# Kernel optimization log

Measured on AMD Instinct MI355X. Metric: run time of the kernel, lower is better.

Reference implementation:

```python
import jax, jax.numpy as jnp
import numpy as np
from jax import lax

EPS = 1e-4  # BatchNorm2d eps
K, STRIDE, PAD = 3, 1, 1


def _conv_nchw(x, w, stride, pad):
    return lax.conv_general_dilated(
        x, w, window_strides=(stride, stride), padding=[(pad, pad), (pad, pad)],
        dimension_numbers=("NCHW", "OIHW", "NCHW"))


def setup_inputs() -> dict:
    key = jax.random.key(0)
    ks = jax.random.split(key, 6)
    N, C, H, W = 16, 256, 56, 56
    Cout = 256
    return {
        "x": jax.random.normal(ks[0], (N, C, H, W), jnp.float32),
        "bn_gamma": jax.random.uniform(ks[1], (C,), jnp.float32, 0.5, 1.5),
        "bn_beta": jax.random.normal(ks[2], (C,), jnp.float32) * 0.1,
        "conv_w": jax.random.normal(ks[3], (Cout, C, K, K), jnp.float32) * (1.0 / np.sqrt(C * K * K)),
        "conv_b": jax.random.normal(ks[4], (Cout,), jnp.float32) * 0.01,
        "beta_conv_b": jax.random.normal(ks[5], (1,), jnp.float32) * 0.01,
    }


def reference(x, bn_gamma, bn_beta, conv_w, conv_b, beta_conv_b):
    # --- BatchNorm2d (training-mode batch stats, affine) ---
    mean = jnp.mean(x, axis=(0, 2, 3), keepdims=True)
    var = jnp.mean(jnp.square(x - mean), axis=(0, 2, 3), keepdims=True)  # biased
    xn = (x - mean) * lax.rsqrt(var + EPS)
    xn = xn * bn_gamma[None, :, None, None] + bn_beta[None, :, None, None]

    # --- Ternary quantize (threshold=0; le overwrites ge, so x==0 -> -1) ---
    t = jnp.where(xn >= 0.0, 1.0, 0.0)
    t = jnp.where(xn <= 0.0, -1.0, t).astype(xn.dtype)
    # scale=True, clamp=True
    xc = jnp.clip(xn, -1.0, 1.0)
    c_sum = jnp.sum(xc * t, axis=1, keepdims=True)       # [N,1,H,W]
    c_cnt = jnp.sum(jnp.abs(t), axis=1, keepdims=True)   # L1 norm over channels

    # --- Main conv on ternary activations ---
    y = _conv_nchw(t, conv_w, STRIDE, PAD) + conv_b[None, :, None, None]

    # --- beta: ones-weight box filter (+ beta_conv bias) ---
    ones_k = jnp.ones((1, 1, K, K), x.dtype)
    b_sum = _conv_nchw(c_sum, ones_k, STRIDE, PAD) + beta_conv_b[0]
    b_cnt = _conv_nchw(c_cnt, ones_k, STRIDE, PAD) + beta_conv_b[0]
    beta_map = b_sum / b_cnt                             # [N,1,Ho,Wo]
    return y * beta_map
```

## Files before the change

### kernel.cpp

```cpp
#include <hip/hip_runtime.h>
#include <hip/hip_bf16.h>

typedef __attribute__((ext_vector_type(8))) short bf16x8;
typedef __attribute__((ext_vector_type(4))) float f32x4;

#define NB 16
#define C 256
#define HH 56
#define WW 56
#define HW 3136
#define CHW 802816
#define NPIX 50176
#define PH 58
#define PW 58
#define KTOT 2304
#define PPI 3364
#define NPIXP 53824

#define GLL(g, l) __builtin_amdgcn_global_load_lds( \
    (const __attribute__((address_space(1))) void*)(g), \
    (__attribute__((address_space(3))) void*)(l), 16, 0, 0)

__global__ __launch_bounds__(1024) void stats_kernel(const float* __restrict__ x,
                             const float* __restrict__ gamma, double* __restrict__ stats) {
  int c = blockIdx.x, tid = threadIdx.x;
  double s = 0.0, s2 = 0.0;
  const float* xc = x + (size_t)c * HW;
  for (int k = tid; k < NB * (HW / 4); k += 1024) {
    int n = k / (HW / 4), i = k - n * (HW / 4);
    float4 v = *(const float4*)(xc + (size_t)n * CHW + i * 4);
    double a = v.x, b = v.y, cc = v.z, d = v.w;
    s  += (a + b) + (cc + d);
    s2 += (a * a + b * b) + (cc * cc + d * d);
  }
  __shared__ double rs[1024], rq[1024];
  rs[tid] = s; rq[tid] = s2; __syncthreads();
  for (int o = 512; o > 0; o >>= 1) {
    if (tid < o) { rs[tid] += rs[tid + o]; rq[tid] += rq[tid + o]; }
    __syncthreads();
  }
  if (tid == 0) {
    double mean = rs[0] / (double)NPIX;
    double var = rq[0] / (double)NPIX - mean * mean;
    stats[c] = mean;
    stats[C + c] = (double)gamma[c] / sqrt(var + 1e-4);
  }
}

__global__ __launch_bounds__(256) void ternarize_kernel(const float* __restrict__ x,
                                 const float* __restrict__ beta,
                                 const double* __restrict__ stats,
                                 unsigned short* __restrict__ Tp, float* __restrict__ csum) {
  int bid = blockIdx.x, tid = threadIdx.x;
  int n = bid / HH, h = bid - n * HH;
  __shared__ float xs[256][57];
  const float* xb = x + (size_t)n * CHW + h * WW;
#pragma unroll
  for (int j = 0; j < 14; ++j) {
    int idx = j * 256 + tid;
    int c = idx / 14, q = idx - c * 14;
    float4 v = *(const float4*)(xb + (size_t)c * HW + q * 4);
    float* row = &xs[c][q * 4];
    row[0] = v.x; row[1] = v.y; row[2] = v.z; row[3] = v.w;
  }
  int c8 = tid & 31;
  double mu[8], sc[8], bt[8];
#pragma unroll
  for (int e = 0; e < 8; ++e) {
    int c = c8 + 32 * e;
    mu[e] = stats[c]; sc[e] = stats[C + c]; bt[e] = (double)beta[c];
  }
  __syncthreads();
  unsigned short* tb = Tp + ((size_t)(n * PH + h + 1) * PW + 1) * C;
  float* cs = csum + (size_t)(n * PH + h + 1) * PW + 1;
#pragma unroll
  for (int p = 0; p < 7; ++p) {
    int idx = p * 256 + tid;
    int w = idx >> 5;
    unsigned bits[4];
    float msum = 0.f;
#pragma unroll
    for (int e2 = 0; e2 < 4; ++e2) {
      unsigned lo, hi;
      {
        double xn = ((double)xs[c8 + 64 * e2][w] - mu[2 * e2]) * sc[2 * e2] + bt[2 * e2];
        lo = (xn > 0.0) ? 0x3F80u : 0xBF80u;
        msum += (float)fmin(fabs(xn), 1.0);
      }
      {
        double xn = ((double)xs[c8 + 64 * e2 + 32][w] - mu[2 * e2 + 1]) * sc[2 * e2 + 1] + bt[2 * e2 + 1];
        hi = (xn > 0.0) ? 0x3F80u : 0xBF80u;
        msum += (float)fmin(fabs(xn), 1.0);
      }
      bits[e2] = lo | (hi << 16);
    }
    msum += __shfl_xor(msum, 1); msum += __shfl_xor(msum, 2);
    msum += __shfl_xor(msum, 4); msum += __shfl_xor(msum, 8);
    msum += __shfl_xor(msum, 16);
    uint4 v4; v4.x = bits[0]; v4.y = bits[1]; v4.z = bits[2]; v4.w = bits[3];
    *(uint4*)(tb + (size_t)w * C + c8 * 8) = v4;
    if (c8 == 0) cs[w] = msum;
  }
}

__global__ void prep_kernel(const float* __restrict__ cw, unsigned short* __restrict__ Wp,
                            unsigned short* __restrict__ Tp, float* __restrict__ csum) {
  int b = blockIdx.x, tid = threadIdx.x;
  if (b < 2304) {
    int o = b * 256 + tid;
    int co = o / KTOT, rr = o - co * KTOT;
    int tap = rr >> 8, p = rr & 255;
    int c = (p & 7) * 32 + (p >> 3);
    float v = cw[co * KTOT + c * 9 + tap];
    unsigned u = __builtin_bit_cast(unsigned, v);
    unsigned lsb = (u >> 16) & 1u;
    u += 0x7FFFu + lsb;
    Wp[o] = (unsigned short)(u >> 16);
  } else if (b < 2760) {
    int g = (b - 2304) * 256 + tid;
    if (g >= 16 * 228 * 32) return;
    int n = g / 7296; int r = g - n * 7296;
    int pix = r >> 5, c8 = r & 31;
    int h, w;
    if (pix < 58)      { h = 0;  w = pix; }
    else if (pix < 116){ h = 57; w = pix - 58; }
    else { int rem = pix - 116; h = 1 + (rem >> 1); w = (rem & 1) ? 57 : 0; }
    uint4 z = {0u, 0u, 0u, 0u};
    *(uint4*)(Tp + (size_t)((n * PH + h) * PW + w) * C + c8 * 8) = z;
  } else {
    int i = (b - 2760) * 256 + tid;
    if (i < NPIXP) csum[i] = 0.f;
  }
}

__global__ void betamap_kernel(const float* __restrict__ csum, const float* __restrict__ betab,
                               float* __restrict__ bmap) {
  int idx = blockIdx.x * 256 + threadIdx.x;
  if (idx >= NPIX) return;
  int n = idx / HW, r = idx - n * HW;
  int h = r / WW, w = r - h * WW;
  const float* p = csum + (size_t)(n * PH + h) * PW + w;
  float s = 0.f;
  for (int i = 0; i < 3; ++i)
    for (int j = 0; j < 3; ++j) s += p[i * PW + j];
  int rows = 3 - (h == 0) - (h == HH - 1);
  int cols = 3 - (w == 0) - (w == WW - 1);
  float bb = betab[0];
  bmap[idx] = (s + bb) / (256.0f * (float)(rows * cols) + bb);
}

__global__ __launch_bounds__(256) void conv_kernel(const unsigned short* __restrict__ Wp,
    const unsigned short* __restrict__ Tp, const float* __restrict__ convb,
    const float* __restrict__ bmap, float* __restrict__ out) {
  int bid = blockIdx.x;
  int ptg = bid >> 5, xcd = bid & 7, ct = (bid >> 3) & 3;
  int pt = ptg * 8 + xcd;
  if (pt >= 211) return;
  int tid = threadIdx.x;
  int co0 = ct * 64;

  __shared__ __align__(16) unsigned short As[3 * 64 * 32];
  __shared__ __align__(16) unsigned short Bs[320 * 32];

  size_t aofs[3];
#pragma unroll
  for (int r = 0; r < 3; ++r) {
    int lin = r * 256 + tid;
    int co = (lin >> 2) & 63, tap3 = lin >> 8, pseg = lin & 3;
    int lseg = pseg ^ ((co >> 1) & 3);
    aofs[r] = (size_t)(co0 + co) * KTOT + tap3 * 256 + lseg * 8;
  }
  int bpix[5], blseg[5];
#pragma unroll
  for (int r = 0; r < 5; ++r) {
    int lin = r * 256 + tid;
    bpix[r] = lin >> 2;
    blseg[r] = (lin & 3) ^ ((bpix[r] >> 1) & 3);
  }

  int lane = tid & 63, wid = tid >> 6;
  int quad = lane >> 4, row16 = lane & 15;
  int aperm = (quad ^ ((row16 >> 1) & 3)) * 8;
  const unsigned short* aF = As + row16 * 32 + aperm;
  int jbase = wid * 64 + row16 + 31;

  f32x4 acc[4][4];
#pragma unroll
  for (int mi = 0; mi < 4; ++mi)
#pragma unroll
    for (int ni = 0; ni < 4; ++ni)
      acc[mi][ni] = (f32x4){0.f, 0.f, 0.f, 0.f};

  for (int kh = 0; kh < 3; ++kh) {
    int wbase = pt * 256 + (kh - 1) * 58 - 32;
    size_t bofs[5];
#pragma unroll
    for (int r = 0; r < 5; ++r) {
      int q = wbase + bpix[r];
      q = q < 0 ? 0 : (q >= NPIXP ? NPIXP - 1 : q);
      bofs[r] = (size_t)q * C + blseg[r] * 8;
    }
    size_t akh = (size_t)kh * 768;
    for (int c0 = 0; c0 < 256; c0 += 32) {
      __syncthreads();
#pragma unroll
      for (int r = 0; r < 3; ++r) GLL(Wp + aofs[r] + akh + c0, As + (r * 256 + tid) * 8);
#pragma unroll
      for (int r = 0; r < 5; ++r) GLL(Tp + bofs[r] + c0, Bs + (r * 256 + tid) * 8);
      __syncthreads();
#pragma unroll
      for (int kw = 0; kw < 3; ++kw) {
        bf16x8 a[4], b[4];
#pragma unroll
        for (int mi = 0; mi < 4; ++mi)
          a[mi] = *(const bf16x8*)(aF + kw * 2048 + mi * 512);
#pragma unroll
        for (int ni = 0; ni < 4; ++ni) {
          int pix = jbase + ni * 16 + kw;
          b[ni] = *(const bf16x8*)(Bs + pix * 32 + ((quad ^ ((pix >> 1) & 3)) * 8));
        }
#pragma unroll
        for (int mi = 0; mi < 4; ++mi)
#pragma unroll
          for (int ni = 0; ni < 4; ++ni)
            acc[mi][ni] = __builtin_amdgcn_mfma_f32_16x16x32_bf16(a[mi], b[ni], acc[mi][ni], 0, 0, 0);
      }
    }
  }

#pragma unroll
  for (int ni = 0; ni < 4; ++ni) {
    int pp = pt * 256 + wid * 64 + ni * 16 + row16;
    if (pp >= NPIXP) continue;
    int n = pp / PPI; int r = pp - n * PPI;
    int ph = r / PW;  int pw = r - ph * PW;
    if (ph < 1 || ph > 56 || pw < 1 || pw > 56) continue;
    int pix = (ph - 1) * WW + (pw - 1);
    float bm = bmap[n * HW + pix];
    float* ob = out + (size_t)n * CHW + pix;
#pragma unroll
    for (int mi = 0; mi < 4; ++mi) {
      int co = co0 + mi * 16 + quad * 4;
#pragma unroll
      for (int rg = 0; rg < 4; ++rg) {
        ob[(size_t)(co + rg) * HW] = (acc[mi][ni][rg] + convb[co + rg]) * bm;
      }
    }
  }
}

extern "C" void kernel_launch(void* const* d_in, const int* in_sizes, int n_in,
                              void* d_out, int out_size, void* d_ws, size_t ws_size,
                              hipStream_t stream) {
  const float* x     = (const float*)d_in[0];
  const float* gamma = (const float*)d_in[1];
  const float* beta  = (const float*)d_in[2];
  const float* convw = (const float*)d_in[3];
  const float* convb = (const float*)d_in[4];
  const float* betab = (const float*)d_in[5];
  float* out = (float*)d_out;

  char* ws = (char*)d_ws;
  unsigned short* Tp   = (unsigned short*)(ws);
  unsigned short* Wp   = (unsigned short*)(ws + 27557888);
  float*          csum = (float*)(ws + 28737536);
  float*          bmap = (float*)(ws + 28952832);
  double*         stats= (double*)(ws + 29153536);

  prep_kernel<<<2971, 256, 0, stream>>>(convw, Wp, Tp, csum);
  stats_kernel<<<256, 1024, 0, stream>>>(x, gamma, stats);
  ternarize_kernel<<<896, 256, 0, stream>>>(x, beta, stats, Tp, csum);
  betamap_kernel<<<196, 256, 0, stream>>>(csum, betab, bmap);
  conv_kernel<<<864, 256, 0, stream>>>(Wp, Tp, convb, bmap, out);
}
```

Baseline: 203.8 us.

## Stage all nine taps per channel chunk, sharing one padded pixel window across kh

```diff
diff --git a/kernel.cpp b/kernel.cpp
--- a/kernel.cpp
+++ b/kernel.cpp
@@ -106,19 +106,23 @@
 __global__ void prep_kernel(const float* __restrict__ cw, unsigned short* __restrict__ Wp,
                             unsigned short* __restrict__ Tp, float* __restrict__ csum) {
   int b = blockIdx.x, tid = threadIdx.x;
-  if (b < 2304) {
-    int o = b * 256 + tid;
-    int co = o / KTOT, rr = o - co * KTOT;
-    int tap = rr >> 8, p = rr & 255;
-    int c = (p & 7) * 32 + (p >> 3);
-    float v = cw[co * KTOT + c * 9 + tap];
-    unsigned u = __builtin_bit_cast(unsigned, v);
-    unsigned lsb = (u >> 16) & 1u;
-    u += 0x7FFFu + lsb;
-    Wp[o] = (unsigned short)(u >> 16);
-  } else if (b < 2760) {
-    int g = (b - 2304) * 256 + tid;
-    if (g >= 16 * 228 * 32) return;
+  if (b < 256) {
+    int co = b;
+    const float* src = cw + (size_t)co * KTOT;
+    unsigned short* dst = Wp + (size_t)co * KTOT;
+    float v[9];
+#pragma unroll
+    for (int t9 = 0; t9 < 9; ++t9) v[t9] = src[tid * 9 + t9];
+    int p = (tid & 31) * 8 + (tid >> 5);
+#pragma unroll
+    for (int t9 = 0; t9 < 9; ++t9) {
+      unsigned u = __builtin_bit_cast(unsigned, v[t9]);
+      unsigned lsb = (u >> 16) & 1u;
+      u += 0x7FFFu + lsb;
+      dst[t9 * 256 + p] = (unsigned short)(u >> 16);
+    }
+  } else if (b < 712) {
+    int g = (b - 256) * 256 + tid;
     int n = g / 7296; int r = g - n * 7296;
     int pix = r >> 5, c8 = r & 31;
     int h, w;
@@ -128,7 +132,7 @@
     uint4 z = {0u, 0u, 0u, 0u};
     *(uint4*)(Tp + (size_t)((n * PH + h) * PW + w) * C + c8 * 8) = z;
   } else {
-    int i = (b - 2760) * 256 + tid;
+    int i = (b - 712) * 256 + tid;
     if (i < NPIXP) csum[i] = 0.f;
   }
 }
@@ -159,30 +163,34 @@
   int tid = threadIdx.x;
   int co0 = ct * 64;
 
-  __shared__ __align__(16) unsigned short As[3 * 64 * 32];
-  __shared__ __align__(16) unsigned short Bs[320 * 32];
-
-  size_t aofs[3];
-#pragma unroll
-  for (int r = 0; r < 3; ++r) {
+  __shared__ __align__(16) unsigned short As[9 * 64 * 32];
+  __shared__ __align__(16) unsigned short Bs[384 * 32];
+
+  int aofs[9];
+#pragma unroll
+  for (int r = 0; r < 9; ++r) {
     int lin = r * 256 + tid;
-    int co = (lin >> 2) & 63, tap3 = lin >> 8, pseg = lin & 3;
+    int co = (lin >> 2) & 63, tap = lin >> 8, pseg = lin & 3;
     int lseg = pseg ^ ((co >> 1) & 3);
-    aofs[r] = (size_t)(co0 + co) * KTOT + tap3 * 256 + lseg * 8;
-  }
-  int bpix[5], blseg[5];
-#pragma unroll
-  for (int r = 0; r < 5; ++r) {
+    aofs[r] = (co0 + co) * KTOT + tap * 256 + lseg * 8;
+  }
+  int wstart = pt * 256 - 59;
+  int bofs[6];
+#pragma unroll
+  for (int r = 0; r < 6; ++r) {
     int lin = r * 256 + tid;
-    bpix[r] = lin >> 2;
-    blseg[r] = (lin & 3) ^ ((bpix[r] >> 1) & 3);
+    int bpix = lin >> 2, pseg = lin & 3;
+    int lseg = pseg ^ ((bpix >> 1) & 3);
+    int q = wstart + bpix;
+    q = q < 0 ? 0 : (q >= NPIXP ? NPIXP - 1 : q);
+    bofs[r] = q * C + lseg * 8;
   }
 
   int lane = tid & 63, wid = tid >> 6;
   int quad = lane >> 4, row16 = lane & 15;
   int aperm = (quad ^ ((row16 >> 1) & 3)) * 8;
   const unsigned short* aF = As + row16 * 32 + aperm;
-  int jbase = wid * 64 + row16 + 31;
+  int pixb = wid * 64 + row16;
 
   f32x4 acc[4][4];
 #pragma unroll
@@ -191,32 +199,26 @@
     for (int ni = 0; ni < 4; ++ni)
       acc[mi][ni] = (f32x4){0.f, 0.f, 0.f, 0.f};
 
-  for (int kh = 0; kh < 3; ++kh) {
-    int wbase = pt * 256 + (kh - 1) * 58 - 32;
-    size_t bofs[5];
-#pragma unroll
-    for (int r = 0; r < 5; ++r) {
-      int q = wbase + bpix[r];
-      q = q < 0 ? 0 : (q >= NPIXP ? NPIXP - 1 : q);
-      bofs[r] = (size_t)q * C + blseg[r] * 8;
-    }
-    size_t akh = (size_t)kh * 768;
-    for (int c0 = 0; c0 < 256; c0 += 32) {
-      __syncthreads();
-#pragma unroll
-      for (int r = 0; r < 3; ++r) GLL(Wp + aofs[r] + akh + c0, As + (r * 256 + tid) * 8);
-#pragma unroll
-      for (int r = 0; r < 5; ++r) GLL(Tp + bofs[r] + c0, Bs + (r * 256 + tid) * 8);
-      __syncthreads();
+  for (int c0 = 0; c0 < 256; c0 += 32) {
+    __syncthreads();
+#pragma unroll
+    for (int r = 0; r < 9; ++r) GLL(Wp + aofs[r] + c0, As + (r * 256 + tid) * 8);
+#pragma unroll
+    for (int r = 0; r < 6; ++r) GLL(Tp + bofs[r] + c0, Bs + (r * 256 + tid) * 8);
+    __syncthreads();
+    __builtin_amdgcn_s_setprio(1);
+#pragma unroll
+    for (int kh = 0; kh < 3; ++kh) {
 #pragma unroll
       for (int kw = 0; kw < 3; ++kw) {
+        int tap = kh * 3 + kw;
         bf16x8 a[4], b[4];
 #pragma unroll
         for (int mi = 0; mi < 4; ++mi)
-          a[mi] = *(const bf16x8*)(aF + kw * 2048 + mi * 512);
+          a[mi] = *(const bf16x8*)(aF + tap * 2048 + mi * 512);
 #pragma unroll
         for (int ni = 0; ni < 4; ++ni) {
-          int pix = jbase + ni * 16 + kw;
+          int pix = pixb + ni * 16 + kh * 58 + kw;
           b[ni] = *(const bf16x8*)(Bs + pix * 32 + ((quad ^ ((pix >> 1) & 3)) * 8));
         }
 #pragma unroll
@@ -226,6 +228,7 @@
             acc[mi][ni] = __builtin_amdgcn_mfma_f32_16x16x32_bf16(a[mi], b[ni], acc[mi][ni], 0, 0, 0);
       }
     }
+    __builtin_amdgcn_s_setprio(0);
   }
 
 #pragma unroll
@@ -267,7 +270,7 @@
   float*          bmap = (float*)(ws + 28952832);
   double*         stats= (double*)(ws + 29153536);
 
-  prep_kernel<<<2971, 256, 0, stream>>>(convw, Wp, Tp, csum);
+  prep_kernel<<<923, 256, 0, stream>>>(convw, Wp, Tp, csum);
   stats_kernel<<<256, 1024, 0, stream>>>(x, gamma, stats);
   ternarize_kernel<<<896, 256, 0, stream>>>(x, beta, stats, Tp, csum);
   betamap_kernel<<<196, 256, 0, stream>>>(csum, betab, bmap);
```

Result: faster. 188.6 us (-7.5%).
